# Optimization experiments

Hardware: AMD Instinct MI355X
Metric: run time of the kernel (lower is better)

The kernel has to match this reference:

```python
import jax, jax.numpy as jnp
import numpy as np

DM = 1024        # model dim
NEXPERTS = 32    # experts per set; also group size t for the token permutation
EXPERTSETS = 4
EXPERTSIZE = 32  # dff = NEXPERTS * EXPERTSETS * EXPERTSIZE = 4096
BATCH, SEQ = 4, 2048


def setup_inputs() -> dict:
    key = jax.random.key(0)
    k0, k1, k2, k3 = jax.random.split(key, 4)
    scale = 0.02
    x = jax.random.normal(k0, (BATCH, SEQ, DM), jnp.float32)
    controller = jax.random.normal(k1, (DM, NEXPERTS, EXPERTSETS), jnp.float32) * scale
    f1 = jax.random.normal(k2, (DM, NEXPERTS, EXPERTSETS, EXPERTSIZE), jnp.float32) * scale
    bias = jnp.zeros((NEXPERTS, EXPERTSETS, EXPERTSIZE), jnp.float32)
    f2 = jax.random.normal(k3, (NEXPERTS, EXPERTSETS, EXPERTSIZE, DM), jnp.float32) * scale
    return {"x": x, "controller": controller, "f1": f1, "bias": bias, "f2": f2}


def reference(x, controller, f1, bias, f2):
    B, L, d = x.shape
    t = controller.shape[1]            # nexperts == group size
    g = L // t                         # number of token groups per example
    grouped = x.reshape(B, g, t, d)    # '... (b t) d -> ... b t d'

    # controller logits: '... t d, d e s -> ... t e s'
    logits = jnp.einsum('bgtd,des->bgtes', grouped, controller)
    # deterministic tiebreak over the token axis t (dim -3)
    tie = jnp.linspace(0.0, 1e-6, t, dtype=logits.dtype).reshape(t, 1, 1)
    logits = logits + tie
    # one-hot-ish permutation: for each (e, s) slot pick the argmax token in the group
    perm = (logits == jnp.max(logits, axis=-3, keepdims=True)).astype(x.dtype)
    perm = jax.lax.stop_gradient(perm)  # torch eq() produces detached bool mask

    # einsum 1 ('... t d, d e s f, ... t e s -> ... e s f'), done in the efficient order:
    # dispatch tokens to expert slots first, then the per-expert GEMM
    dispatched = jnp.einsum('bgtd,bgtes->bgesd', grouped, perm)
    inner = jax.nn.relu(jnp.einsum('bgesd,desf->bgesf', dispatched, f1) + bias)

    # einsum 2 + unpermute
    intermediate = jnp.einsum('bgesf,esfd->bgesd', inner, f2)
    out = jnp.einsum('bgesd,bgtes->bgtd', intermediate, perm)

    return out.reshape(B, L, d)
```

## Files before the change

kernel.cpp:

```cpp
#include <hip/hip_runtime.h>
#include <hip/hip_bf16.h>

#define NGROUP 256
#define NSLOT  128
#define TG     32
#define DM     1024
#define FF     32

#define LSCALE     4096.0f
#define INV_LSCALE (1.0f / 4096.0f)

typedef unsigned int  uint;
typedef unsigned short ushort;
typedef unsigned char uchar;
typedef __attribute__((ext_vector_type(4))) float f32x4;
typedef __attribute__((ext_vector_type(8))) short bf16x8;
typedef __attribute__((ext_vector_type(8))) _Float16 f16x8;

__device__ __forceinline__ ushort f2bf(float f) {
    uint u = __float_as_uint(f);
    u += 0x7FFFu + ((u >> 16) & 1u);
    return (ushort)(u >> 16);
}
__device__ __forceinline__ uint pk2(float a, float b) {
    return (uint)f2bf(a) | ((uint)f2bf(b) << 16);
}

__device__ __forceinline__ void gload_lds16(const void* g, void* l) {
    __builtin_amdgcn_global_load_lds(
        (const __attribute__((address_space(1))) uint*)g,
        (__attribute__((address_space(3))) uint*)l, 16, 0, 0);
}

__global__ __launch_bounds__(256) void k_fused1(
    const float* __restrict__ x, const float* __restrict__ ctrl,
    const float* __restrict__ f1, const float* __restrict__ f2,
    int* __restrict__ idx, uchar* __restrict__ idx8, ushort* __restrict__ xb,
    ushort* __restrict__ f1F, ushort* __restrict__ f2T)
{
    __shared__ float smem[4 * 32 * 64];
    const int t = threadIdx.x;

    if (blockIdx.x < 512) {
        float* Lp = smem;
        const int g  = blockIdx.x >> 1;
        const int nh = blockIdx.x & 1;
        const int w = t >> 6;
        const int lane = t & 63;
        const int lrow = lane & 15;
        const int lk8 = (lane >> 4) * 8;

        const size_t xoff0 = ((size_t)g * TG + lrow) * DM + w * 256 + lk8;
        const float* xr0 = x + xoff0;
        const float* xr1 = xr0 + 16 * DM;

        f32x4 ahh[2][4], ax[2][4];
#pragma unroll
        for (int mt = 0; mt < 2; ++mt)
#pragma unroll
            for (int nt = 0; nt < 4; ++nt) {
                ahh[mt][nt] = (f32x4){0.f, 0.f, 0.f, 0.f};
                ax[mt][nt]  = (f32x4){0.f, 0.f, 0.f, 0.f};
            }

        for (int ks = 0; ks < 8; ++ks) {
            f16x8 Ah[2], Al[2];
#pragma unroll
            for (int mt = 0; mt < 2; ++mt) {
                const float* p = (mt ? xr1 : xr0) + ks * 32;
                float xe[8];
                *(float4*)&xe[0] = *(const float4*)p;
                *(float4*)&xe[4] = *(const float4*)(p + 4);
                union { f16x8 v; _Float16 e[8]; } H, L;
#pragma unroll
                for (int j = 0; j < 8; ++j) {
                    const _Float16 h = (_Float16)xe[j];
                    H.e[j] = h;
                    L.e[j] = (_Float16)((xe[j] - (float)h) * LSCALE);
                }
                Ah[mt] = H.v; Al[mt] = L.v;
                if (nh == 0) {
                    uint4 o;
                    o.x = pk2(xe[0], xe[1]); o.y = pk2(xe[2], xe[3]);
                    o.z = pk2(xe[4], xe[5]); o.w = pk2(xe[6], xe[7]);
                    *(uint4*)(xb + xoff0 + (size_t)mt * 16 * DM + ks * 32) = o;
                }
            }
            const int kslice = w * 8 + ks;
#pragma unroll
            for (int nt = 0; nt < 4; ++nt) {
                const float* cp = ctrl
                    + (size_t)(kslice * 32 + ((lane >> 4) << 3)) * NSLOT
                    + nh * 64 + nt * 16 + (lane & 15);
                union { f16x8 v; _Float16 e[8]; } BH, BL;
#pragma unroll
                for (int j = 0; j < 8; ++j) {
                    const float c = cp[(size_t)j * NSLOT];
                    const _Float16 h = (_Float16)c;
                    BH.e[j] = h;
                    BL.e[j] = (_Float16)((c - (float)h) * LSCALE);
                }
#pragma unroll
                for (int mt = 0; mt < 2; ++mt) {
                    ahh[mt][nt] = __builtin_amdgcn_mfma_f32_16x16x32_f16(Ah[mt], BH.v, ahh[mt][nt], 0, 0, 0);
                    ax[mt][nt]  = __builtin_amdgcn_mfma_f32_16x16x32_f16(Al[mt], BH.v, ax[mt][nt], 0, 0, 0);
                    ax[mt][nt]  = __builtin_amdgcn_mfma_f32_16x16x32_f16(Ah[mt], BL.v, ax[mt][nt], 0, 0, 0);
                }
            }
        }

#pragma unroll
        for (int mt = 0; mt < 2; ++mt)
#pragma unroll
            for (int nt = 0; nt < 4; ++nt)
#pragma unroll
                for (int r = 0; r < 4; ++r) {
                    const int trow = mt * 16 + (lane >> 4) * 4 + r;
                    const int nl = nt * 16 + lrow;
                    Lp[(w * TG + trow) * 64 + nl] =
                        ahh[mt][nt][r] + ax[mt][nt][r] * INV_LSCALE;
                }
        __syncthreads();

        for (int i = t * 4; i < TG * 64; i += 256 * 4) {
            f32x4 s0 = *(const f32x4*)&Lp[i];
            f32x4 s1 = *(const f32x4*)&Lp[2048 + i];
            f32x4 s2 = *(const f32x4*)&Lp[4096 + i];
            f32x4 s3 = *(const f32x4*)&Lp[6144 + i];
            *(f32x4*)&Lp[i] = (s0 + s1) + (s2 + s3);
        }
        __syncthreads();

        if (t < 64) {
            const int n = t;
            float best = -1e30f;
            int bi = 0;
#pragma unroll
            for (int tt = 0; tt < TG; ++tt) {
                const float v = Lp[tt * 64 + n] + (float)tt * (1e-6f / 31.0f);
                if (v >= best) { best = v; bi = tt; }
            }
            idx[g * NSLOT + nh * 64 + n] = bi;
            idx8[g * NSLOT + nh * 64 + n] = (uchar)bi;
        }
    } else if (blockIdx.x < 768) {
        float* Ltr = smem;
        const int i1 = blockIdx.x - 512;
        const int es = i1 >> 1;
        const int dh = i1 & 1;
        for (int d0 = dh * 512; d0 < dh * 512 + 512; d0 += 64) {
            const int dd = t >> 2, f0 = (t & 3) * 8;
            const float* src = f1 + (size_t)(d0 + dd) * 4096 + es * FF + f0;
            float4 a = *(const float4*)src;
            float4 b = *(const float4*)(src + 4);
            __syncthreads();
            float* Lq = &Ltr[dd * 33 + f0];
            Lq[0] = a.x; Lq[1] = a.y; Lq[2] = a.z; Lq[3] = a.w;
            Lq[4] = b.x; Lq[5] = b.y; Lq[6] = b.z; Lq[7] = b.w;
            __syncthreads();
            const int f = t & 31, koct = t >> 5;
            const int nt = f >> 4;
            const int kg = d0 + koct * 8;
            const int kslice = kg >> 5;
            const int lane2 = (f & 15) | (((kg >> 3) & 3) << 4);
            uint4 o;
            o.x = pk2(Ltr[(koct * 8 + 0) * 33 + f], Ltr[(koct * 8 + 1) * 33 + f]);
            o.y = pk2(Ltr[(koct * 8 + 2) * 33 + f], Ltr[(koct * 8 + 3) * 33 + f]);
            o.z = pk2(Ltr[(koct * 8 + 4) * 33 + f], Ltr[(koct * 8 + 5) * 33 + f]);
            o.w = pk2(Ltr[(koct * 8 + 6) * 33 + f], Ltr[(koct * 8 + 7) * 33 + f]);
            *(uint4*)(f1F + ((((size_t)es * 2 + nt) * 32 + kslice) * 64 + lane2) * 8) = o;
        }
    } else {
        float* Ltr = smem;
        const int i2 = blockIdx.x - 768;
        const int es = i2 >> 2;
        const int dq = i2 & 3;
        for (int d0 = dq * 256; d0 < dq * 256 + 256; d0 += 64) {
            const int f = t >> 3, ds = (t & 7) * 8;
            const float* src = f2 + (size_t)es * (FF * DM) + f * DM + d0 + ds;
            float4 a = *(const float4*)src;
            float4 b = *(const float4*)(src + 4);
            __syncthreads();
            Ltr[(ds + 0) * 33 + f] = a.x; Ltr[(ds + 1) * 33 + f] = a.y;
            Ltr[(ds + 2) * 33 + f] = a.z; Ltr[(ds + 3) * 33 + f] = a.w;
            Ltr[(ds + 4) * 33 + f] = b.x; Ltr[(ds + 5) * 33 + f] = b.y;
            Ltr[(ds + 6) * 33 + f] = b.z; Ltr[(ds + 7) * 33 + f] = b.w;
            __syncthreads();
            const int dd = t >> 2, f0 = (t & 3) * 8;
            uint4 o;
            o.x = pk2(Ltr[dd * 33 + f0 + 0], Ltr[dd * 33 + f0 + 1]);
            o.y = pk2(Ltr[dd * 33 + f0 + 2], Ltr[dd * 33 + f0 + 3]);
            o.z = pk2(Ltr[dd * 33 + f0 + 4], Ltr[dd * 33 + f0 + 5]);
            o.w = pk2(Ltr[dd * 33 + f0 + 6], Ltr[dd * 33 + f0 + 7]);
            *(uint4*)(f2T + (size_t)es * (FF * DM) + (d0 + dd) * FF + f0) = o;
        }
    }
}

__global__ __launch_bounds__(256) void k_h_mfma(
    const ushort* __restrict__ xb, const ushort* __restrict__ f1F,
    const float* __restrict__ bias, const int* __restrict__ idx,
    ushort* __restrict__ Hb)
{
    const int es = blockIdx.x >> 2;
    const int gq = blockIdx.x & 3;
    const int w = threadIdx.x >> 6;
    const int lane = threadIdx.x & 63;
    const int lrow = lane & 15;
    const int lk8 = (lane >> 4) * 8;

    const int ga = gq * 64 + w * 16 + lrow;
    const int tok = idx[ga * NSLOT + es];
    const ushort* abase = xb + ((size_t)ga * TG + tok) * DM + lk8;
    const ushort* bbase = f1F + (size_t)es * 2 * 32 * 512 + (size_t)lane * 8;

    f32x4 acc[2] = {(f32x4){0.f, 0.f, 0.f, 0.f}, (f32x4){0.f, 0.f, 0.f, 0.f}};

#pragma unroll 4
    for (int kslice = 0; kslice < 32; ++kslice) {
        const bf16x8 A = *(const bf16x8*)(abase + kslice * 32);
#pragma unroll
        for (int nt = 0; nt < 2; ++nt) {
            const bf16x8 B = *(const bf16x8*)(bbase + ((size_t)nt * 32 + kslice) * 512);
            acc[nt] = __builtin_amdgcn_mfma_f32_16x16x32_bf16(A, B, acc[nt], 0, 0, 0);
        }
    }

#pragma unroll
    for (int nt = 0; nt < 2; ++nt) {
        const int f = nt * 16 + lrow;
        const float bv = bias[es * FF + f];
#pragma unroll
        for (int r = 0; r < 4; ++r) {
            const int g = gq * 64 + w * 16 + (lane >> 4) * 4 + r;
            const float hv = fmaxf(acc[nt][r] + bv, 0.0f);
            Hb[(size_t)g * (NSLOT * FF) + es * FF + f] = f2bf(hv);
        }
    }
}

__global__ __launch_bounds__(256) void k_out_mfma(
    const ushort* __restrict__ Hb, const ushort* __restrict__ f2T,
    const uchar* __restrict__ idx8, float* __restrict__ out)
{
    extern __shared__ char smK3[];
    float*  OL    = (float*)smK3;
    char*   Bfull = smK3 + 65536;
    char*   Aring = smK3 + 131072;

    const int db = ((blockIdx.x & 7) << 1) | ((blockIdx.x >> 3) & 1);
    const int go = blockIdx.x >> 4;
    const int G0 = go * 8;
    const int D0 = db * 64;
    const int tid = threadIdx.x;
    const int w = tid >> 6;
    const int lane = tid & 63;
    const int gl = lane & 15;
    const int g8 = gl & 7;
    const int lk8 = (lane >> 4) * 8;

    for (int i = tid * 4; i < 8 * 2048; i += 1024)
        *(f32x4*)&OL[i] = (f32x4){0.f, 0.f, 0.f, 0.f};
#pragma unroll
    for (int it = 0; it < 16; ++it) {
        const int v8 = (tid + it * 256) * 8;
        const int gr = v8 >> 12;
        const int rem = v8 & 4095;
        const int s = rem >> 3;
        const uint4 q = *(const uint4*)(Hb + (size_t)(G0 + gr) * (NSLOT * FF) + rem);
        *(uint4*)(Bfull + gr * 8192 + ((s ^ gr) << 4)) = q;
    }
    uint ui[32];
    {
        const uint4* p = (const uint4*)(idx8 + (size_t)(G0 + g8) * NSLOT);
#pragma unroll
        for (int k = 0; k < 8; ++k) {
            const uint4 v = p[k];
            ui[k * 4 + 0] = v.x; ui[k * 4 + 1] = v.y;
            ui[k * 4 + 2] = v.z; ui[k * 4 + 3] = v.w;
        }
    }
    __syncthreads();

    const ushort* ap = f2T + (size_t)(D0 + w * 16 + gl) * FF + lk8;
    char* ring = Aring + w * 8192;

#pragma unroll
    for (int s = 0; s < 3; ++s) {
        gload_lds16(ap + (size_t)(2 * s)     * (FF * DM), ring + s * 2048);
        gload_lds16(ap + (size_t)(2 * s + 1) * (FF * DM), ring + s * 2048 + 1024);
    }

    float* olrow = &OL[g8 * 2048];
    const int qbase = w * 4 + (lane >> 4);
    const char* bfrow = Bfull + g8 * 8192;
    const int sq = lk8 >> 3;

#pragma unroll
    for (int c = 0; c < 64; ++c) {
        const int sl = (c + 3) & 3;
        const int e2 = ((c + 3) & 63) * 2;
        gload_lds16(ap + (size_t)e2       * (FF * DM), ring + sl * 2048);
        gload_lds16(ap + (size_t)(e2 + 1) * (FF * DM), ring + sl * 2048 + 1024);
        asm volatile("s_waitcnt vmcnt(6)" ::: "memory");

        const char* slot = ring + (c & 3) * 2048;
#pragma unroll
        for (int h = 0; h < 2; ++h) {
            const int e = c * 2 + h;
            const bf16x8 afr = *(const bf16x8*)(slot + h * 1024 + lane * 16);
            const int sB = e * 4 + sq;
            const bf16x8 bfr = *(const bf16x8*)(bfrow + ((sB ^ g8) << 4));
            const f32x4 d = __builtin_amdgcn_mfma_f32_16x16x32_bf16(
                afr, bfr, (f32x4){0.f, 0.f, 0.f, 0.f}, 0, 0, 0);
            const uint tv = (ui[e >> 2] >> ((e & 3) * 8)) & 0xFFu;
            const int q = (int)tv * 16 + qbase;
            float* olp = olrow + ((q ^ g8) << 2);
            *(f32x4*)olp = *(const f32x4*)olp + d;
        }
    }
    asm volatile("s_waitcnt vmcnt(0)" ::: "memory");
    __syncthreads();

    for (int it = 0; it < 16; ++it) {
        const int flat = tid * 4 + it * 1024;
        const int gli = flat >> 11, rem = flat & 2047;
        const int t = rem >> 6, d = rem & 63;
        const int q = rem >> 2;
        const f32x4 v = *(const f32x4*)&OL[gli * 2048 + ((q ^ gli) << 2)];
        *(f32x4*)&out[((size_t)(G0 + gli) * TG + t) * DM + D0 + d] = v;
    }
}

extern "C" void kernel_launch(void* const* d_in, const int* in_sizes, int n_in,
                              void* d_out, int out_size, void* d_ws, size_t ws_size,
                              hipStream_t stream) {
    (void)in_sizes; (void)n_in; (void)out_size; (void)ws_size;
    const float* x    = (const float*)d_in[0];
    const float* ctrl = (const float*)d_in[1];
    const float* f1   = (const float*)d_in[2];
    const float* bias = (const float*)d_in[3];
    const float* f2   = (const float*)d_in[4];
    float* out = (float*)d_out;

    char* ws = (char*)d_ws;
    int*    idx  = (int*)ws;
    ushort* Hb   = (ushort*)(ws + 131072);
    ushort* f1F  = (ushort*)(ws + 2228224);
    ushort* f2T  = (ushort*)(ws + 10616832);
    ushort* xb   = (ushort*)(ws + 19005440);
    uchar*  idx8 = (uchar*)(ws + 35782656);

    k_fused1<<<1280, 256, 0, stream>>>(x, ctrl, f1, f2, idx, idx8, xb, f1F, f2T);

    k_h_mfma<<<NSLOT * 4, 256, 0, stream>>>(xb, f1F, bias, idx, Hb);

    const size_t lds3 = 163840;
    hipFuncSetAttribute((const void*)k_out_mfma,
                        hipFuncAttributeMaxDynamicSharedMemorySize, (int)lds3);
    k_out_mfma<<<512, 256, lds3, stream>>>(Hb, f2T, idx8, out);
}
```

Measured before the change: 84.35 us.

## Stream Hb tiles through per-wave async ring instead of full LDS preload

```diff
diff --git a/kernel.cpp b/kernel.cpp
--- a/kernel.cpp
+++ b/kernel.cpp
@@ -244,11 +244,10 @@
     const uchar* __restrict__ idx8, float* __restrict__ out)
 {
     extern __shared__ char smK3[];
-    float*  OL    = (float*)smK3;
-    char*   Bfull = smK3 + 65536;
-    char*   Aring = smK3 + 131072;
-
-    const int db = ((blockIdx.x & 7) << 1) | ((blockIdx.x >> 3) & 1);
+    float* OL   = (float*)smK3;
+    char*  Ring = smK3 + 65536;
+
+    const int db = blockIdx.x & 15;
     const int go = blockIdx.x >> 4;
     const int G0 = go * 8;
     const int D0 = db * 64;
@@ -257,19 +256,11 @@
     const int lane = tid & 63;
     const int gl = lane & 15;
     const int g8 = gl & 7;
-    const int lk8 = (lane >> 4) * 8;
+    const int sq = lane >> 4;
+    const int lk8 = sq * 8;
 
     for (int i = tid * 4; i < 8 * 2048; i += 1024)
         *(f32x4*)&OL[i] = (f32x4){0.f, 0.f, 0.f, 0.f};
-#pragma unroll
-    for (int it = 0; it < 16; ++it) {
-        const int v8 = (tid + it * 256) * 8;
-        const int gr = v8 >> 12;
-        const int rem = v8 & 4095;
-        const int s = rem >> 3;
-        const uint4 q = *(const uint4*)(Hb + (size_t)(G0 + gr) * (NSLOT * FF) + rem);
-        *(uint4*)(Bfull + gr * 8192 + ((s ^ gr) << 4)) = q;
-    }
     uint ui[32];
     {
         const uint4* p = (const uint4*)(idx8 + (size_t)(G0 + g8) * NSLOT);
@@ -283,34 +274,38 @@
     __syncthreads();
 
     const ushort* ap = f2T + (size_t)(D0 + w * 16 + gl) * FF + lk8;
-    char* ring = Aring + w * 8192;
-
-#pragma unroll
-    for (int s = 0; s < 3; ++s) {
-        gload_lds16(ap + (size_t)(2 * s)     * (FF * DM), ring + s * 2048);
-        gload_lds16(ap + (size_t)(2 * s + 1) * (FF * DM), ring + s * 2048 + 1024);
+    const int beo = lane >> 5, bsq = (lane >> 3) & 3, bg = lane & 7;
+    const ushort* bps = Hb + (size_t)(G0 + bg) * (NSLOT * FF) + beo * FF + bsq * 8;
+    char* ring = Ring + w * 24576;
+
+#pragma unroll
+    for (int s = 0; s < 7; ++s) {
+        char* slot = ring + s * 3072;
+        gload_lds16(ap + (size_t)(2 * s)     * (FF * DM), slot);
+        gload_lds16(ap + (size_t)(2 * s + 1) * (FF * DM), slot + 1024);
+        gload_lds16(bps + (size_t)(2 * s) * FF,           slot + 2048);
     }
 
     float* olrow = &OL[g8 * 2048];
-    const int qbase = w * 4 + (lane >> 4);
-    const char* bfrow = Bfull + g8 * 8192;
-    const int sq = lk8 >> 3;
+    const int qbase = w * 4 + sq;
 
 #pragma unroll
     for (int c = 0; c < 64; ++c) {
-        const int sl = (c + 3) & 3;
-        const int e2 = ((c + 3) & 63) * 2;
-        gload_lds16(ap + (size_t)e2       * (FF * DM), ring + sl * 2048);
-        gload_lds16(ap + (size_t)(e2 + 1) * (FF * DM), ring + sl * 2048 + 1024);
-        asm volatile("s_waitcnt vmcnt(6)" ::: "memory");
-
-        const char* slot = ring + (c & 3) * 2048;
+        {
+            const int cn = (c + 7) & 63;
+            char* slot = ring + ((c + 7) & 7) * 3072;
+            gload_lds16(ap + (size_t)(2 * cn)     * (FF * DM), slot);
+            gload_lds16(ap + (size_t)(2 * cn + 1) * (FF * DM), slot + 1024);
+            gload_lds16(bps + (size_t)(2 * cn) * FF,           slot + 2048);
+        }
+        asm volatile("s_waitcnt vmcnt(21)" ::: "memory");
+
+        const char* slot = ring + (c & 7) * 3072;
 #pragma unroll
         for (int h = 0; h < 2; ++h) {
             const int e = c * 2 + h;
             const bf16x8 afr = *(const bf16x8*)(slot + h * 1024 + lane * 16);
-            const int sB = e * 4 + sq;
-            const bf16x8 bfr = *(const bf16x8*)(bfrow + ((sB ^ g8) << 4));
+            const bf16x8 bfr = *(const bf16x8*)(slot + 2048 + (h * 32 + sq * 8 + g8) * 16);
             const f32x4 d = __builtin_amdgcn_mfma_f32_16x16x32_bf16(
                 afr, bfr, (f32x4){0.f, 0.f, 0.f, 0.f}, 0, 0, 0);
             const uint tv = (ui[e >> 2] >> ((e & 3) * 8)) & 0xFFu;
```

After: 85.45 us. No clear change (+1.3%).
